# Optimization experiments

Measured on AMD Instinct MI355X. Metric: run time of the kernel, lower is better.

The kernel has to match this reference:

```python
import jax, jax.numpy as jnp
import numpy as np

DECAY = 0.99
EPS = 1e-05
DIM = 512
N_EMBED = 4096
B, H, W = 32, 32, 32


def setup_inputs() -> dict:
    key = jax.random.key(0)
    k1, k2, k3, k4, k5 = jax.random.split(key, 5)
    inp = jax.random.normal(k1, (B, H, W, DIM), dtype=jnp.float32)
    labels = jax.random.randint(k2, (B * H * W,), 0, N_EMBED)
    embed = jax.random.normal(k3, (DIM, N_EMBED), dtype=jnp.float32)
    cluster_size = jax.random.uniform(k4, (N_EMBED,), dtype=jnp.float32)
    embed_avg = jax.random.normal(k5, (DIM, N_EMBED), dtype=jnp.float32)
    return {"input": inp, "labels": labels, "embed": embed,
            "cluster_size": cluster_size, "embed_avg": embed_avg}


def reference(input, labels, embed, cluster_size, embed_avg):
    dim, n_embed = embed.shape
    flatten = input.reshape(-1, dim)                      # [N, dim]

    # codebook gather (F.embedding on embed.T)
    embed_ind = labels.reshape(input.shape[:-1])          # [B, H, W]
    quantize = jnp.take(embed.T, embed_ind, axis=0)       # [B, H, W, dim]

    # training EMA update: onehot-scatter expressed as segment_sum
    # (math identical to flatten.T @ one_hot(labels))
    onehot_sum = jnp.zeros((n_embed,), flatten.dtype).at[labels].add(1.0)   # [n_embed]
    embed_sum = jax.ops.segment_sum(flatten, labels, num_segments=n_embed).T  # [dim, n_embed]

    new_cluster_size = cluster_size * DECAY + (1.0 - DECAY) * onehot_sum
    new_embed_avg = embed_avg * DECAY + (1.0 - DECAY) * embed_sum
    n = new_cluster_size.sum()
    cs = (new_cluster_size + EPS) / (n + n_embed * EPS) * n
    new_embed = new_embed_avg / cs[None, :]

    diff = jnp.mean((jax.lax.stop_gradient(quantize) - input) ** 2)
    return (quantize, diff, embed_ind, new_embed, new_cluster_size, new_embed_avg)
```

## Files before the change

### kernel.cpp

```cpp
#include <hip/hip_runtime.h>

#define DIMV   512
#define NEMB   4096
#define NTOK   32768
#define TOTAL  (NTOK * DIMV)

#define OFF_Q    0u
#define OFF_DIFF 16777216u
#define OFF_IND  16777217u
#define OFF_NE   16809985u
#define OFF_NCS  18907137u
#define OFF_NEA  18911233u

#define WS_SUMT    0u
#define WS_BINCNT  2097152u
#define WS_BINST   2101248u
#define WS_CURSOR  2105344u
#define WS_SORTED  2109440u
#define WS_DIFF    2142208u
#define WS_NSUM    2142209u

#define DECAYF 0.99f
#define OMDF   0.01f
#define EPSF   1e-5f

__global__ void k_hist(const int* __restrict__ labels,
                       float* __restrict__ out,
                       int* __restrict__ bin_count) {
    int n = blockIdx.x * 256 + threadIdx.x;
    int lab = labels[n];
    out[OFF_IND + n] = (float)lab;
    atomicAdd(&bin_count[lab], 1);
}

__global__ void k_scan(const int* __restrict__ bin_count,
                       int* __restrict__ bin_start,
                       int* __restrict__ cursor) {
    __shared__ int part[256];
    int t = threadIdx.x;
    int base = t * 16;
    int local[16];
    int s = 0;
    for (int i = 0; i < 16; ++i) { local[i] = s; s += bin_count[base + i]; }
    part[t] = s;
    __syncthreads();
    for (int o = 1; o < 256; o <<= 1) {
        int v = (t >= o) ? part[t - o] : 0;
        __syncthreads();
        part[t] += v;
        __syncthreads();
    }
    int offset = (t == 0) ? 0 : part[t - 1];
    for (int i = 0; i < 16; ++i) {
        int bs = offset + local[i];
        bin_start[base + i] = bs;
        cursor[base + i]    = bs;
    }
}

__global__ void k_scatter(const int* __restrict__ labels,
                          int* __restrict__ cursor,
                          int* __restrict__ sorted_tok) {
    int n = blockIdx.x * 256 + threadIdx.x;
    int lab = labels[n];
    int pos = atomicAdd(&cursor[lab], 1);
    sorted_tok[pos] = n;
}

__global__ __launch_bounds__(256) void k_perlabel(
        const float* __restrict__ inp,
        const float* __restrict__ embed,
        const int*   __restrict__ sorted_tok,
        const int*   __restrict__ bin_start,
        const int*   __restrict__ bin_count,
        float* __restrict__ out,
        float* __restrict__ sumT,
        float* __restrict__ diff_acc) {
    int e = blockIdx.x;
    int t = threadIdx.x;
    int d0 = 2 * t;
    float q0 = embed[(size_t)d0 * NEMB + e];
    float q1 = embed[(size_t)(d0 + 1) * NEMB + e];
    int start = bin_start[e];
    int cnt   = bin_count[e];
    float s0 = 0.f, s1 = 0.f, dacc = 0.f;
    for (int i = 0; i < cnt; ++i) {
        int n = sorted_tok[start + i];
        const float2 x2 = *(const float2*)(inp + (size_t)n * DIMV + d0);
        s0 += x2.x; s1 += x2.y;
        float t0 = q0 - x2.x, t1 = q1 - x2.y;
        dacc += t0 * t0 + t1 * t1;
        *(float2*)(out + OFF_Q + (size_t)n * DIMV + d0) = make_float2(q0, q1);
    }
    *(float2*)(sumT + (size_t)e * DIMV + d0) = make_float2(s0, s1);
    __shared__ float sh[256];
    sh[t] = dacc;
    __syncthreads();
    for (int o = 128; o > 0; o >>= 1) {
        if (t < o) sh[t] += sh[t + o];
        __syncthreads();
    }
    if (t == 0) atomicAdd(diff_acc, sh[0]);
}

__global__ void k_cluster(const float* __restrict__ cluster_size,
                          const int*   __restrict__ bin_count,
                          const float* __restrict__ diff_acc,
                          float* __restrict__ out,
                          float* __restrict__ n_sum) {
    unsigned e = blockIdx.x * 256u + threadIdx.x;
    float ncs = cluster_size[e] * DECAYF + OMDF * (float)bin_count[e];
    out[OFF_NCS + e] = ncs;
    __shared__ float s[256];
    s[threadIdx.x] = ncs;
    __syncthreads();
    for (int o = 128; o > 0; o >>= 1) {
        if ((int)threadIdx.x < o) s[threadIdx.x] += s[threadIdx.x + o];
        __syncthreads();
    }
    if (threadIdx.x == 0) atomicAdd(n_sum, s[0]);
    if (blockIdx.x == 0 && threadIdx.x == 0)
        out[OFF_DIFF] = diff_acc[0] * (1.0f / (float)TOTAL);
}

__global__ __launch_bounds__(256) void k_trans_final(
        const float* __restrict__ embed_avg,
        const float* __restrict__ sumT,
        const float* __restrict__ n_sum,
        float* __restrict__ out) {
    __shared__ float tile[32][33];
    int tx = threadIdx.x & 31;
    int ty = threadIdx.x >> 5;
    int e0 = (blockIdx.x & 127) << 5;
    int d0 = (blockIdx.x >> 7) << 5;
    for (int i = 0; i < 4; ++i) {
        int er = ty + i * 8;
        tile[er][tx] = sumT[(size_t)(e0 + er) * DIMV + d0 + tx];
    }
    __syncthreads();
    float nsum = n_sum[0];
    float ncs  = out[OFF_NCS + e0 + tx];
    float cs   = (ncs + EPSF) / (nsum + (float)NEMB * EPSF) * nsum;
    float inv  = 1.0f / cs;
    for (int i = 0; i < 4; ++i) {
        int dr = d0 + ty + i * 8;
        size_t o = (size_t)dr * NEMB + e0 + tx;
        float val = DECAYF * embed_avg[o] + OMDF * tile[tx][ty + i * 8];
        out[OFF_NEA + o] = val;
        out[OFF_NE + o]  = val * inv;
    }
}

extern "C" void kernel_launch(void* const* d_in, const int* in_sizes, int n_in,
                              void* d_out, int out_size, void* d_ws, size_t ws_size,
                              hipStream_t stream) {
    const float* inp          = (const float*)d_in[0];
    const int*   labels       = (const int*)  d_in[1];
    const float* embed        = (const float*)d_in[2];
    const float* cluster_size = (const float*)d_in[3];
    const float* embed_avg    = (const float*)d_in[4];
    float* out = (float*)d_out;

    float* wsf        = (float*)d_ws;
    float* sumT       = wsf + WS_SUMT;
    int*   bin_count  = (int*)(wsf + WS_BINCNT);
    int*   bin_start  = (int*)(wsf + WS_BINST);
    int*   cursor     = (int*)(wsf + WS_CURSOR);
    int*   sorted_tok = (int*)(wsf + WS_SORTED);
    float* diff_acc   = wsf + WS_DIFF;
    float* n_sum      = wsf + WS_NSUM;

    hipMemsetAsync(wsf + WS_BINCNT, 0, (WS_NSUM - WS_BINCNT + 1) * sizeof(float), stream);

    k_hist      <<<128,  256, 0, stream>>>(labels, out, bin_count);
    k_scan      <<<1,    256, 0, stream>>>(bin_count, bin_start, cursor);
    k_scatter   <<<128,  256, 0, stream>>>(labels, cursor, sorted_tok);
    k_perlabel  <<<4096, 256, 0, stream>>>(inp, embed, sorted_tok, bin_start,
                                           bin_count, out, sumT, diff_acc);
    k_cluster   <<<16,   256, 0, stream>>>(cluster_size, bin_count, diff_acc, out, n_sum);
    k_trans_final<<<2048,256, 0, stream>>>(embed_avg, sumT, n_sum, out);
}
```

Before: 215.4 us.

## Fuse histogram/scan/scatter into single-block sort and widen per-label token loop

Replaces the memset, histogram, scan, scatter and cluster kernels with one 1024-thread single-block kernel that builds the histogram in shared memory, scans it, computes new cluster sizes and their sum, and scatters token indices. The per-label kernel now has each of its four waves handle a different token with float4 loads covering eight dims per lane, staging token indices in shared memory and reducing partial sums across waves. The diff scalar write moves into the final transpose kernel. This cuts launch count and exposes more memory-level parallelism per label, at the cost of a serial single-block sort stage.

```diff
diff --git a/kernel.cpp b/kernel.cpp
--- a/kernel.cpp
+++ b/kernel.cpp
@@ -15,58 +15,96 @@
 #define WS_SUMT    0u
 #define WS_BINCNT  2097152u
 #define WS_BINST   2101248u
-#define WS_CURSOR  2105344u
-#define WS_SORTED  2109440u
-#define WS_DIFF    2142208u
-#define WS_NSUM    2142209u
+#define WS_SORTED  2105344u
+#define WS_DIFF    2138112u
+#define WS_NSUM    2138113u
 
 #define DECAYF 0.99f
 #define OMDF   0.01f
 #define EPSF   1e-5f
 
-__global__ void k_hist(const int* __restrict__ labels,
-                       float* __restrict__ out,
-                       int* __restrict__ bin_count) {
-    int n = blockIdx.x * 256 + threadIdx.x;
-    int lab = labels[n];
-    out[OFF_IND + n] = (float)lab;
-    atomicAdd(&bin_count[lab], 1);
-}
-
-__global__ void k_scan(const int* __restrict__ bin_count,
-                       int* __restrict__ bin_start,
-                       int* __restrict__ cursor) {
-    __shared__ int part[256];
+__global__ __launch_bounds__(1024) void k_sort(
+        const int*   __restrict__ labels,
+        const float* __restrict__ cluster_size,
+        float* __restrict__ out,
+        int*   __restrict__ bin_count,
+        int*   __restrict__ bin_start,
+        int*   __restrict__ sorted_tok,
+        float* __restrict__ n_sum,
+        float* __restrict__ diff_acc) {
+    __shared__ int   hist[NEMB];
+    __shared__ int   part[1024];
+    __shared__ float fred[1024];
     int t = threadIdx.x;
-    int base = t * 16;
-    int local[16];
-    int s = 0;
-    for (int i = 0; i < 16; ++i) { local[i] = s; s += bin_count[base + i]; }
-    part[t] = s;
-    __syncthreads();
-    for (int o = 1; o < 256; o <<= 1) {
+    #pragma unroll
+    for (int i = 0; i < 4; ++i) hist[t + i * 1024] = 0;
+    __syncthreads();
+
+    int4 labs[8];
+    #pragma unroll
+    for (int i = 0; i < 8; ++i) {
+        int n4 = (i * 1024 + t) * 4;
+        int4 l = *(const int4*)(labels + n4);
+        labs[i] = l;
+        out[OFF_IND + n4 + 0] = (float)l.x;
+        out[OFF_IND + n4 + 1] = (float)l.y;
+        out[OFF_IND + n4 + 2] = (float)l.z;
+        out[OFF_IND + n4 + 3] = (float)l.w;
+        atomicAdd(&hist[l.x], 1); atomicAdd(&hist[l.y], 1);
+        atomicAdd(&hist[l.z], 1); atomicAdd(&hist[l.w], 1);
+    }
+    __syncthreads();
+
+    int c[4]; int csum = 0; float nl = 0.f;
+    #pragma unroll
+    for (int i = 0; i < 4; ++i) {
+        int b = t * 4 + i;
+        int cc = hist[b];
+        c[i] = csum; csum += cc;
+        bin_count[b] = cc;
+        float ncs = cluster_size[b] * DECAYF + OMDF * (float)cc;
+        out[OFF_NCS + b] = ncs;
+        nl += ncs;
+    }
+    part[t] = csum;
+    fred[t] = nl;
+    __syncthreads();
+    for (int o = 1; o < 1024; o <<= 1) {
         int v = (t >= o) ? part[t - o] : 0;
         __syncthreads();
         part[t] += v;
         __syncthreads();
     }
-    int offset = (t == 0) ? 0 : part[t - 1];
-    for (int i = 0; i < 16; ++i) {
-        int bs = offset + local[i];
-        bin_start[base + i] = bs;
-        cursor[base + i]    = bs;
-    }
-}
-
-__global__ void k_scatter(const int* __restrict__ labels,
-                          int* __restrict__ cursor,
-                          int* __restrict__ sorted_tok) {
-    int n = blockIdx.x * 256 + threadIdx.x;
-    int lab = labels[n];
-    int pos = atomicAdd(&cursor[lab], 1);
-    sorted_tok[pos] = n;
-}
-
+    for (int o = 512; o > 0; o >>= 1) {
+        if (t < o) fred[t] += fred[t + o];
+        __syncthreads();
+    }
+    if (t == 0) { n_sum[0] = fred[0]; diff_acc[0] = 0.f; }
+
+    int base = part[t] - csum;
+    int bs[4];
+    #pragma unroll
+    for (int i = 0; i < 4; ++i) {
+        bs[i] = base + c[i];
+        bin_start[t * 4 + i] = bs[i];
+    }
+    __syncthreads();
+    #pragma unroll
+    for (int i = 0; i < 4; ++i) hist[t * 4 + i] = bs[i];
+    __syncthreads();
+
+    #pragma unroll
+    for (int i = 0; i < 8; ++i) {
+        int n4 = (i * 1024 + t) * 4;
+        int4 l = labs[i];
+        sorted_tok[atomicAdd(&hist[l.x], 1)] = n4 + 0;
+        sorted_tok[atomicAdd(&hist[l.y], 1)] = n4 + 1;
+        sorted_tok[atomicAdd(&hist[l.z], 1)] = n4 + 2;
+        sorted_tok[atomicAdd(&hist[l.w], 1)] = n4 + 3;
+    }
+}
+
+#define CHUNK 128
 __global__ __launch_bounds__(256) void k_perlabel(
         const float* __restrict__ inp,
         const float* __restrict__ embed,
@@ -76,23 +114,62 @@
         float* __restrict__ out,
         float* __restrict__ sumT,
         float* __restrict__ diff_acc) {
-    int e = blockIdx.x;
-    int t = threadIdx.x;
-    int d0 = 2 * t;
-    float q0 = embed[(size_t)d0 * NEMB + e];
-    float q1 = embed[(size_t)(d0 + 1) * NEMB + e];
+    int e    = blockIdx.x;
+    int t    = threadIdx.x;
+    int wave = t >> 6;
+    int lane = t & 63;
+    int d0   = lane << 3;
+
+    float qa0 = embed[(size_t)(d0 + 0) * NEMB + e];
+    float qa1 = embed[(size_t)(d0 + 1) * NEMB + e];
+    float qa2 = embed[(size_t)(d0 + 2) * NEMB + e];
+    float qa3 = embed[(size_t)(d0 + 3) * NEMB + e];
+    float qb0 = embed[(size_t)(d0 + 4) * NEMB + e];
+    float qb1 = embed[(size_t)(d0 + 5) * NEMB + e];
+    float qb2 = embed[(size_t)(d0 + 6) * NEMB + e];
+    float qb3 = embed[(size_t)(d0 + 7) * NEMB + e];
+    float4 qa = make_float4(qa0, qa1, qa2, qa3);
+    float4 qb = make_float4(qb0, qb1, qb2, qb3);
+
     int start = bin_start[e];
     int cnt   = bin_count[e];
-    float s0 = 0.f, s1 = 0.f, dacc = 0.f;
-    for (int i = 0; i < cnt; ++i) {
-        int n = sorted_tok[start + i];
-        const float2 x2 = *(const float2*)(inp + (size_t)n * DIMV + d0);
-        s0 += x2.x; s1 += x2.y;
-        float t0 = q0 - x2.x, t1 = q1 - x2.y;
-        dacc += t0 * t0 + t1 * t1;
-        *(float2*)(out + OFF_Q + (size_t)n * DIMV + d0) = make_float2(q0, q1);
-    }
-    *(float2*)(sumT + (size_t)e * DIMV + d0) = make_float2(s0, s1);
+
+    __shared__ int toks[CHUNK];
+    float4 sa = make_float4(0, 0, 0, 0);
+    float4 sb = make_float4(0, 0, 0, 0);
+    float dacc = 0.f;
+
+    for (int base = 0; base < cnt; base += CHUNK) {
+        int m = min(CHUNK, cnt - base);
+        if (t < m) toks[t] = sorted_tok[start + base + t];
+        __syncthreads();
+        #pragma unroll 2
+        for (int i = wave; i < m; i += 4) {
+            int n = toks[i];
+            const float* row = inp + (size_t)n * DIMV + d0;
+            float4 xa = *(const float4*)(row);
+            float4 xb = *(const float4*)(row + 4);
+            sa.x += xa.x; sa.y += xa.y; sa.z += xa.z; sa.w += xa.w;
+            sb.x += xb.x; sb.y += xb.y; sb.z += xb.z; sb.w += xb.w;
+            float t0 = qa.x - xa.x, t1 = qa.y - xa.y, t2 = qa.z - xa.z, t3 = qa.w - xa.w;
+            float u0 = qb.x - xb.x, u1 = qb.y - xb.y, u2 = qb.z - xb.z, u3 = qb.w - xb.w;
+            dacc += t0 * t0 + t1 * t1 + t2 * t2 + t3 * t3
+                  + u0 * u0 + u1 * u1 + u2 * u2 + u3 * u3;
+            float* orow = out + OFF_Q + (size_t)n * DIMV + d0;
+            *(float4*)(orow)     = qa;
+            *(float4*)(orow + 4) = qb;
+        }
+        __syncthreads();
+    }
+
+    __shared__ float ssum[4][DIMV];
+    *(float4*)(&ssum[wave][d0])     = sa;
+    *(float4*)(&ssum[wave][d0 + 4]) = sb;
+    __syncthreads();
+    for (int d = t; d < DIMV; d += 256) {
+        sumT[(size_t)e * DIMV + d] =
+            ssum[0][d] + ssum[1][d] + ssum[2][d] + ssum[3][d];
+    }
     __shared__ float sh[256];
     sh[t] = dacc;
     __syncthreads();
@@ -101,32 +178,13 @@
         __syncthreads();
     }
     if (t == 0) atomicAdd(diff_acc, sh[0]);
-}
-
-__global__ void k_cluster(const float* __restrict__ cluster_size,
-                          const int*   __restrict__ bin_count,
-                          const float* __restrict__ diff_acc,
-                          float* __restrict__ out,
-                          float* __restrict__ n_sum) {
-    unsigned e = blockIdx.x * 256u + threadIdx.x;
-    float ncs = cluster_size[e] * DECAYF + OMDF * (float)bin_count[e];
-    out[OFF_NCS + e] = ncs;
-    __shared__ float s[256];
-    s[threadIdx.x] = ncs;
-    __syncthreads();
-    for (int o = 128; o > 0; o >>= 1) {
-        if ((int)threadIdx.x < o) s[threadIdx.x] += s[threadIdx.x + o];
-        __syncthreads();
-    }
-    if (threadIdx.x == 0) atomicAdd(n_sum, s[0]);
-    if (blockIdx.x == 0 && threadIdx.x == 0)
-        out[OFF_DIFF] = diff_acc[0] * (1.0f / (float)TOTAL);
 }
 
 __global__ __launch_bounds__(256) void k_trans_final(
         const float* __restrict__ embed_avg,
         const float* __restrict__ sumT,
         const float* __restrict__ n_sum,
+        const float* __restrict__ diff_acc,
         float* __restrict__ out) {
     __shared__ float tile[32][33];
     int tx = threadIdx.x & 31;
@@ -149,6 +207,8 @@
         out[OFF_NEA + o] = val;
         out[OFF_NE + o]  = val * inv;
     }
+    if (blockIdx.x == 0 && threadIdx.x == 0)
+        out[OFF_DIFF] = diff_acc[0] * (1.0f / (float)TOTAL);
 }
 
 extern "C" void kernel_launch(void* const* d_in, const int* in_sizes, int n_in,
@@ -165,18 +225,14 @@
     float* sumT       = wsf + WS_SUMT;
     int*   bin_count  = (int*)(wsf + WS_BINCNT);
     int*   bin_start  = (int*)(wsf + WS_BINST);
-    int*   cursor     = (int*)(wsf + WS_CURSOR);
     int*   sorted_tok = (int*)(wsf + WS_SORTED);
     float* diff_acc   = wsf + WS_DIFF;
     float* n_sum      = wsf + WS_NSUM;
 
-    hipMemsetAsync(wsf + WS_BINCNT, 0, (WS_NSUM - WS_BINCNT + 1) * sizeof(float), stream);
-
-    k_hist      <<<128,  256, 0, stream>>>(labels, out, bin_count);
-    k_scan      <<<1,    256, 0, stream>>>(bin_count, bin_start, cursor);
-    k_scatter   <<<128,  256, 0, stream>>>(labels, cursor, sorted_tok);
-    k_perlabel  <<<4096, 256, 0, stream>>>(inp, embed, sorted_tok, bin_start,
-                                           bin_count, out, sumT, diff_acc);
-    k_cluster   <<<16,   256, 0, stream>>>(cluster_size, bin_count, diff_acc, out, n_sum);
-    k_trans_final<<<2048,256, 0, stream>>>(embed_avg, sumT, n_sum, out);
-}
+    k_sort      <<<1,    1024, 0, stream>>>(labels, cluster_size, out,
+                                            bin_count, bin_start, sorted_tok,
+                                            n_sum, diff_acc);
+    k_perlabel  <<<4096, 256,  0, stream>>>(inp, embed, sorted_tok, bin_start,
+                                            bin_count, out, sumT, diff_acc);
+    k_trans_final<<<2048,256,  0, stream>>>(embed_avg, sumT, n_sum, diff_acc, out);
+}
```

Result: slower. 231.7 us (+7.6%).

## Use one wave per label with batched float4 loads, fold cluster stats into scan

Applied to the files above, without the earlier changes.

The per-label kernel now gives each label one 64-lane wave instead of a 256-thread block. Each lane handles 8 dims with float4 loads, preloads token indices and broadcasts them by shuffle, and issues 8 row loads at once to raise memory-level parallelism. The diff reduction becomes a wave shuffle with one atomic per wave instead of a shared-memory tree. The cluster-size update and n_sum reduction move into the single-block scan kernel, the diff finalisation moves into the transpose kernel, and the memset becomes a small zero kernel. This removes one launch, but the extra serial work in the scan block may add latency.

```diff
diff --git a/kernel.cpp b/kernel.cpp
--- a/kernel.cpp
+++ b/kernel.cpp
@@ -33,16 +33,34 @@
     atomicAdd(&bin_count[lab], 1);
 }
 
+__global__ void k_zero(int* __restrict__ bin_count, float* __restrict__ diff_acc) {
+    int i = blockIdx.x * 256 + threadIdx.x;
+    bin_count[i] = 0;
+    if (i == 0) diff_acc[0] = 0.f;
+}
+
 __global__ void k_scan(const int* __restrict__ bin_count,
+                       const float* __restrict__ cluster_size,
                        int* __restrict__ bin_start,
-                       int* __restrict__ cursor) {
-    __shared__ int part[256];
+                       int* __restrict__ cursor,
+                       float* __restrict__ out,
+                       float* __restrict__ n_sum) {
+    __shared__ int   part[256];
+    __shared__ float fred[256];
     int t = threadIdx.x;
     int base = t * 16;
-    int local[16];
-    int s = 0;
-    for (int i = 0; i < 16; ++i) { local[i] = s; s += bin_count[base + i]; }
+    int loc[16];
+    int s = 0; float nl = 0.f;
+    #pragma unroll
+    for (int i = 0; i < 16; ++i) {
+        int cc = bin_count[base + i];
+        loc[i] = s; s += cc;
+        float ncs = cluster_size[base + i] * DECAYF + OMDF * (float)cc;
+        out[OFF_NCS + base + i] = ncs;
+        nl += ncs;
+    }
     part[t] = s;
+    fred[t] = nl;
     __syncthreads();
     for (int o = 1; o < 256; o <<= 1) {
         int v = (t >= o) ? part[t - o] : 0;
@@ -50,11 +68,16 @@
         part[t] += v;
         __syncthreads();
     }
-    int offset = (t == 0) ? 0 : part[t - 1];
+    for (int o = 128; o > 0; o >>= 1) {
+        if (t < o) fred[t] += fred[t + o];
+        __syncthreads();
+    }
+    if (t == 0) n_sum[0] = fred[0];
+    int off = (t == 0) ? 0 : part[t - 1];
+    #pragma unroll
     for (int i = 0; i < 16; ++i) {
-        int bs = offset + local[i];
-        bin_start[base + i] = bs;
-        cursor[base + i]    = bs;
+        bin_start[base + i] = off + loc[i];
+        cursor[base + i]    = off + loc[i];
     }
 }
 
@@ -76,57 +99,82 @@
         float* __restrict__ out,
         float* __restrict__ sumT,
         float* __restrict__ diff_acc) {
-    int e = blockIdx.x;
-    int t = threadIdx.x;
-    int d0 = 2 * t;
-    float q0 = embed[(size_t)d0 * NEMB + e];
-    float q1 = embed[(size_t)(d0 + 1) * NEMB + e];
+    int t    = threadIdx.x;
+    int wave = t >> 6;
+    int lane = t & 63;
+    int e    = (blockIdx.x << 2) | wave;
+    int d0   = lane << 3;
+
+    const float* col = embed + e;
+    float4 qa, qb;
+    qa.x = col[(size_t)(d0 + 0) * NEMB];
+    qa.y = col[(size_t)(d0 + 1) * NEMB];
+    qa.z = col[(size_t)(d0 + 2) * NEMB];
+    qa.w = col[(size_t)(d0 + 3) * NEMB];
+    qb.x = col[(size_t)(d0 + 4) * NEMB];
+    qb.y = col[(size_t)(d0 + 5) * NEMB];
+    qb.z = col[(size_t)(d0 + 6) * NEMB];
+    qb.w = col[(size_t)(d0 + 7) * NEMB];
+
     int start = bin_start[e];
     int cnt   = bin_count[e];
-    float s0 = 0.f, s1 = 0.f, dacc = 0.f;
-    for (int i = 0; i < cnt; ++i) {
-        int n = sorted_tok[start + i];
-        const float2 x2 = *(const float2*)(inp + (size_t)n * DIMV + d0);
-        s0 += x2.x; s1 += x2.y;
-        float t0 = q0 - x2.x, t1 = q1 - x2.y;
-        dacc += t0 * t0 + t1 * t1;
-        *(float2*)(out + OFF_Q + (size_t)n * DIMV + d0) = make_float2(q0, q1);
-    }
-    *(float2*)(sumT + (size_t)e * DIMV + d0) = make_float2(s0, s1);
-    __shared__ float sh[256];
-    sh[t] = dacc;
-    __syncthreads();
-    for (int o = 128; o > 0; o >>= 1) {
-        if (t < o) sh[t] += sh[t + o];
-        __syncthreads();
-    }
-    if (t == 0) atomicAdd(diff_acc, sh[0]);
-}
-
-__global__ void k_cluster(const float* __restrict__ cluster_size,
-                          const int*   __restrict__ bin_count,
-                          const float* __restrict__ diff_acc,
-                          float* __restrict__ out,
-                          float* __restrict__ n_sum) {
-    unsigned e = blockIdx.x * 256u + threadIdx.x;
-    float ncs = cluster_size[e] * DECAYF + OMDF * (float)bin_count[e];
-    out[OFF_NCS + e] = ncs;
-    __shared__ float s[256];
-    s[threadIdx.x] = ncs;
-    __syncthreads();
-    for (int o = 128; o > 0; o >>= 1) {
-        if ((int)threadIdx.x < o) s[threadIdx.x] += s[threadIdx.x + o];
-        __syncthreads();
-    }
-    if (threadIdx.x == 0) atomicAdd(n_sum, s[0]);
-    if (blockIdx.x == 0 && threadIdx.x == 0)
-        out[OFF_DIFF] = diff_acc[0] * (1.0f / (float)TOTAL);
+
+    float4 sa = make_float4(0, 0, 0, 0);
+    float4 sb = make_float4(0, 0, 0, 0);
+    float dacc = 0.f;
+
+    for (int base = 0; base < cnt; base += 64) {
+        int m = min(64, cnt - base);
+        int idx = (lane < m) ? sorted_tok[start + base + lane] : 0;
+        for (int sub = 0; sub < m; sub += 8) {
+            int mm = min(8, m - sub);
+            int n[8];
+            float4 xa[8], xb[8];
+            #pragma unroll
+            for (int j = 0; j < 8; ++j) {
+                if (j < mm) {
+                    n[j] = __shfl(idx, sub + j);
+                    const float4* r =
+                        (const float4*)(inp + (size_t)n[j] * DIMV + d0);
+                    xa[j] = r[0];
+                    xb[j] = r[1];
+                }
+            }
+            #pragma unroll
+            for (int j = 0; j < 8; ++j) {
+                if (j < mm) {
+                    sa.x += xa[j].x; sa.y += xa[j].y;
+                    sa.z += xa[j].z; sa.w += xa[j].w;
+                    sb.x += xb[j].x; sb.y += xb[j].y;
+                    sb.z += xb[j].z; sb.w += xb[j].w;
+                    float t0 = qa.x - xa[j].x, t1 = qa.y - xa[j].y;
+                    float t2 = qa.z - xa[j].z, t3 = qa.w - xa[j].w;
+                    float u0 = qb.x - xb[j].x, u1 = qb.y - xb[j].y;
+                    float u2 = qb.z - xb[j].z, u3 = qb.w - xb[j].w;
+                    dacc += t0 * t0 + t1 * t1 + t2 * t2 + t3 * t3
+                          + u0 * u0 + u1 * u1 + u2 * u2 + u3 * u3;
+                    float4* orow =
+                        (float4*)(out + OFF_Q + (size_t)n[j] * DIMV + d0);
+                    orow[0] = qa;
+                    orow[1] = qb;
+                }
+            }
+        }
+    }
+
+    float* so = sumT + (size_t)e * DIMV + d0;
+    *(float4*)(so)     = sa;
+    *(float4*)(so + 4) = sb;
+
+    for (int o = 32; o > 0; o >>= 1) dacc += __shfl_down(dacc, o);
+    if (lane == 0) atomicAdd(diff_acc, dacc);
 }
 
 __global__ __launch_bounds__(256) void k_trans_final(
         const float* __restrict__ embed_avg,
         const float* __restrict__ sumT,
         const float* __restrict__ n_sum,
+        const float* __restrict__ diff_acc,
         float* __restrict__ out) {
     __shared__ float tile[32][33];
     int tx = threadIdx.x & 31;
@@ -149,6 +197,8 @@
         out[OFF_NEA + o] = val;
         out[OFF_NE + o]  = val * inv;
     }
+    if (blockIdx.x == 0 && threadIdx.x == 0)
+        out[OFF_DIFF] = diff_acc[0] * (1.0f / (float)TOTAL);
 }
 
 extern "C" void kernel_launch(void* const* d_in, const int* in_sizes, int n_in,
@@ -170,13 +220,12 @@
     float* diff_acc   = wsf + WS_DIFF;
     float* n_sum      = wsf + WS_NSUM;
 
-    hipMemsetAsync(wsf + WS_BINCNT, 0, (WS_NSUM - WS_BINCNT + 1) * sizeof(float), stream);
-
+    k_zero      <<<16,   256, 0, stream>>>(bin_count, diff_acc);
     k_hist      <<<128,  256, 0, stream>>>(labels, out, bin_count);
-    k_scan      <<<1,    256, 0, stream>>>(bin_count, bin_start, cursor);
+    k_scan      <<<1,    256, 0, stream>>>(bin_count, cluster_size, bin_start,
+                                           cursor, out, n_sum);
     k_scatter   <<<128,  256, 0, stream>>>(labels, cursor, sorted_tok);
-    k_perlabel  <<<4096, 256, 0, stream>>>(inp, embed, sorted_tok, bin_start,
+    k_perlabel  <<<1024, 256, 0, stream>>>(inp, embed, sorted_tok, bin_start,
                                            bin_count, out, sumT, diff_acc);
-    k_cluster   <<<16,   256, 0, stream>>>(cluster_size, bin_count, diff_acc, out, n_sum);
-    k_trans_final<<<2048,256, 0, stream>>>(embed_avg, sumT, n_sum, out);
-}
+    k_trans_final<<<2048,256, 0, stream>>>(embed_avg, sumT, n_sum, diff_acc, out);
+}
```

Result: slower. 226.7 us (+5.2%).
